# Performance work log

Hardware: AMD Instinct MI355X
Metric: run time of the kernel (lower is better)

## Reference

```python
import jax, jax.numpy as jnp
import numpy as np


def setup_inputs() -> dict:
    key = jax.random.key(0)
    ks = jax.random.split(key, 6)
    B, T, I, H, O = 64, 512, 256, 512, 256
    stdv = 1.0 / np.sqrt(H)
    u = lambda k, shape: jax.random.uniform(k, shape, jnp.float32, -stdv, stdv)
    return {
        "x": jax.random.normal(ks[0], (B, T, I), jnp.float32),
        "W": u(ks[1], (I, 4 * H)),
        "U": u(ks[2], (H, 4 * H)),
        "bias": u(ks[3], (4 * H,)),
        "Wl": u(ks[4], (H, O)),
        "bl": u(ks[5], (O,)),
    }


def lstm_scan(x, W, U, bias):
    B, T, I = x.shape
    H = U.shape[0]
    # Precompute input projections for all timesteps in one big GEMM: [B,T,4H]
    x_proj = jnp.einsum("bti,ig->btg", x, W) + bias

    def step(carry, xp_t):
        h, c = carry
        gates = xp_t + h @ U  # [B, 4H]
        i_t = jax.nn.sigmoid(gates[:, :H])
        f_t = jax.nn.sigmoid(gates[:, H:2 * H])
        g_t = jnp.tanh(gates[:, 2 * H:3 * H])
        o_t = jax.nn.sigmoid(gates[:, 3 * H:])
        c_new = f_t * c + i_t * g_t
        h_new = o_t * jnp.tanh(c_new)
        return (h_new, c_new), h_new

    h0 = jnp.zeros((B, H), x.dtype)
    c0 = jnp.zeros((B, H), x.dtype)
    (h_T, c_T), hs = jax.lax.scan(step, (h0, c0), jnp.swapaxes(x_proj, 0, 1))
    hidden_seq = jnp.swapaxes(hs, 0, 1)  # [B, T, H]
    return hidden_seq, h_T, c_T


def reference(x, W, U, bias, Wl, bl):
    hidden_seq, h_T, c_T = lstm_scan(x, W, U, bias)
    out = hidden_seq @ Wl + bl  # [B, T, O]
    return out, (h_T, c_T)
```

## Files before the change

### kernel.cpp

```cpp
#include <hip/hip_runtime.h>
#include <stdint.h>

typedef uint16_t u16;
typedef uint32_t u32;
typedef unsigned long long u64;
typedef __attribute__((ext_vector_type(8))) __bf16 bf16x8;
typedef __attribute__((ext_vector_type(8))) short short8;
typedef __attribute__((ext_vector_type(4))) float floatx4;

__device__ __forceinline__ float bf2f(u16 u) {
  union { u32 i; float f; } v; v.i = ((u32)u) << 16; return v.f;
}
__device__ __forceinline__ u16 f2bf(float f) {
  union { float f; u32 i; } v; v.f = f;
  u32 i = v.i;
  return (u16)((i + 0x7FFFu + ((i >> 16) & 1u)) >> 16);
}
__device__ __forceinline__ float sigm(float x) { return 1.f / (1.f + __expf(-x)); }
__device__ __forceinline__ float tanh_f(float x) {
  x = fminf(15.f, fmaxf(-15.f, x));
  float e = __expf(2.f * x);
  return (e - 1.f) / (e + 1.f);
}

__global__ __launch_bounds__(256) void transpose_all(
    const float* __restrict__ W, const float* __restrict__ U,
    const float* __restrict__ Wl,
    u16* __restrict__ WT, u16* __restrict__ UT, u16* __restrict__ WlT) {
  __shared__ u16 tile[32][33];
  int j = blockIdx.x;
  const float* src; u16* dst; int R, C, bx, by;
  if (j < 1024)      { src = U;  dst = UT;  R = 512; C = 2048; bx = j & 63; by = j >> 6; }
  else if (j < 1536) { j -= 1024; src = W;  dst = WT;  R = 256; C = 2048; bx = j & 63; by = j >> 6; }
  else               { j -= 1536; src = Wl; dst = WlT; R = 512; C = 256;  bx = j & 7;  by = j >> 3; }
  const int tx = threadIdx.x & 31, ty = threadIdx.x >> 5;
  int x = bx * 32 + tx;
#pragma unroll
  for (int jj = 0; jj < 4; ++jj) {
    int y = by * 32 + ty + jj * 8;
    tile[ty + jj * 8][tx] = f2bf(src[(size_t)y * C + x]);
  }
  __syncthreads();
  int x2 = by * 32 + tx;
#pragma unroll
  for (int jj = 0; jj < 4; ++jj) {
    int y2 = bx * 32 + ty + jj * 8;
    dst[(size_t)y2 * R + x2] = tile[tx][ty + jj * 8];
  }
}

#define T_STEPS 512
#define HLSZ (16 * 520)
#define NWORK 224

#define LSTM_STEP(XC, XN, TT)                                                  \
  {                                                                            \
    const int t = (TT);                                                        \
    const int tn = (t + 1) & (T_STEPS - 1);                                    \
          \
    if (((tn) & 63) == 0 && t < T_STEPS - 1) {                                 \
      _Pragma("unroll")                                                        \
      for (int r = 0; r < 4; ++r) {                                            \
        const u32* cc = xpctr + ((g * 16 + q4 * 4 + r) * 8 + (tn >> 6));       \
        while (__hip_atomic_load(cc, __ATOMIC_RELAXED,                         \
                                 __HIP_MEMORY_SCOPE_AGENT) < 32u)              \
          __builtin_amdgcn_s_sleep(2);                                         \
      }                                                                        \
      __asm__ volatile("" ::: "memory");                                       \
    }                                                                          \
                   \
    _Pragma("unroll")                                                          \
    for (int qg = 0; qg < 4; ++qg)                                             \
      _Pragma("unroll")                                                        \
      for (int r = 0; r < 4; ++r)                                              \
        XN[qg * 4 + r] = xp_base[((size_t)(q4 * 4 + r) * T_STEPS + tn) * 2048  \
                                 + qg * 512 + cb + n];                         \
    __asm__ volatile("" ::: "memory");                                         \
    floatx4 acc[4] = {};                                                       \
    if (t > 0) {                                                               \
      const u64* hsrc = (const u64*)(hT_all)                                   \
                        + (size_t)(g * T_STEPS + (t - 1)) * 2048;              \
      u64 v[8];                                                                \
      for (;;) {                                                               \
        _Pragma("unroll")                                                      \
        for (int it = 0; it < 8; ++it)                                         \
          v[it] = __hip_atomic_load(hsrc + it * 256 + tid, __ATOMIC_RELAXED,   \
                                    __HIP_MEMORY_SCOPE_AGENT);                 \
        bool ok = true;                                                        \
        _Pragma("unroll")                                                      \
        for (int it = 0; it < 8; ++it) ok &= (v[it] != ~0ull);                 \
        if (ok) break;                                                         \
      }                                                                        \
      __asm__ volatile("" ::: "memory");                                       \
      u16* buf = hls + ((t - 1) & 1) * HLSZ;                                   \
      _Pragma("unroll")                                                        \
      for (int it = 0; it < 8; ++it) {                                         \
        int idx = it * 256 + tid;                                              \
        int tile = idx >> 6, w = idx & 63;                                     \
        *(u64*)(buf + (w >> 2) * 520 + tile * 16 + (w & 3) * 4) = v[it];       \
      }                                                                        \
      __syncthreads();                                                         \
      _Pragma("unroll")                                                        \
      for (int kt = 0; kt < 16; ++kt) {                                        \
        bf16x8 a = *(const bf16x8*)(buf + n * 520 + kt * 32 + q4 * 8);         \
        acc[0] = __builtin_amdgcn_mfma_f32_16x16x32_bf16(a, u[0][kt], acc[0], 0, 0, 0); \
        acc[1] = __builtin_amdgcn_mfma_f32_16x16x32_bf16(a, u[1][kt], acc[1], 0, 0, 0); \
        acc[2] = __builtin_amdgcn_mfma_f32_16x16x32_bf16(a, u[2][kt], acc[2], 0, 0, 0); \
        acc[3] = __builtin_amdgcn_mfma_f32_16x16x32_bf16(a, u[3][kt], acc[3], 0, 0, 0); \
      }                                                                        \
    }                                                                          \
    _Pragma("unroll")                                                          \
    for (int r = 0; r < 4; ++r) {                                              \
      float gi = sigm(acc[0][r] + bf2f(XC[r]));                                \
      float gf = sigm(acc[1][r] + bf2f(XC[4 + r]));                            \
      float gg = tanh_f(acc[2][r] + bf2f(XC[8 + r]));                          \
      float go = sigm(acc[3][r] + bf2f(XC[12 + r]));                           \
      float cn = gf * cst[r] + gi * gg;                                        \
      cst[r] = cn;                                                             \
      float hv = go * tanh_f(cn);                                              \
      int row = q4 * 4 + r;                                                    \
      hp[row * 16 + n] = f2bf(hv);                                             \
      if (t == T_STEPS - 1) {                                                  \
        out_hT[(g * 16 + row) * 512 + cb + n] = hv;                            \
        out_cT[(g * 16 + row) * 512 + cb + n] = cn;                            \
      }                                                                        \
    }                                                                          \
    __asm__ volatile("s_waitcnt lgkmcnt(0)" ::: "memory");                     \
    {                                                                          \
      u64 v = *(const u64*)(hp + (lane >> 2) * 16 + (lane & 3) * 4);           \
      u64* hdst = (u64*)(hT_all) + (size_t)(g * T_STEPS + t) * 2048            \
                  + p * 64 + lane;                                             \
      __hip_atomic_store(hdst, v, __ATOMIC_RELAXED, __HIP_MEMORY_SCOPE_AGENT); \
    }                                                                          \
  }

__global__ __launch_bounds__(256, 1) void fused_lstm(
    const float* __restrict__ x,
    const u16* __restrict__ WT,
    const float* __restrict__ bias,
    u16* __restrict__ xp,
    const u16* __restrict__ UT,
    u16* __restrict__ hT_all,
    const u16* __restrict__ WlT,
    const float* __restrict__ bl,
    float* __restrict__ outC,
    float* __restrict__ out_hT,
    float* __restrict__ out_cT,
    u32* __restrict__ xpctr) {
  __shared__ __align__(16) u16 smem[2 * HLSZ + 4 * 256];
  const int bi = blockIdx.x;
  const int tid = threadIdx.x;

  if (bi >= 32) {
    u16* As = smem;
    u16* Bs = smem + 64 * 40;
    const int wid = bi - 32;
    const int wave = tid >> 6, lane = tid & 63;
    const int q4 = lane >> 4, n16 = lane & 15;
    const int mw = (wave >> 1) * 32, nw = (wave & 1) * 32;
    const int ldrow = tid >> 2, ldseg = (tid & 3) * 8;

    for (int j = wid; j < 16384; j += NWORK) {
      const int tch = j >> 11;
      const int rem = j & 2047;
      const int b = rem >> 5, nt = rem & 31;
      const int m0 = b * 512 + tch * 64, n0 = nt * 64;
      floatx4 acc[2][2] = {};
      for (int k0 = 0; k0 < 256; k0 += 32) {
        const float* ap = x + (size_t)(m0 + ldrow) * 256 + k0 + ldseg;
        floatx4 a0 = *(const floatx4*)ap;
        floatx4 a1 = *(const floatx4*)(ap + 4);
        short8 s;
        s[0] = (short)f2bf(a0[0]); s[1] = (short)f2bf(a0[1]);
        s[2] = (short)f2bf(a0[2]); s[3] = (short)f2bf(a0[3]);
        s[4] = (short)f2bf(a1[0]); s[5] = (short)f2bf(a1[1]);
        s[6] = (short)f2bf(a1[2]); s[7] = (short)f2bf(a1[3]);
        *(short8*)(As + ldrow * 40 + ldseg) = s;
        *(short8*)(Bs + ldrow * 40 + ldseg) =
            *(const short8*)(WT + (size_t)(n0 + ldrow) * 256 + k0 + ldseg);
        __syncthreads();
#pragma unroll
        for (int mi = 0; mi < 2; ++mi) {
          bf16x8 a = *(const bf16x8*)(As + (mw + mi * 16 + n16) * 40 + q4 * 8);
#pragma unroll
          for (int ni = 0; ni < 2; ++ni) {
            bf16x8 bb = *(const bf16x8*)(Bs + (nw + ni * 16 + n16) * 40 + q4 * 8);
            acc[mi][ni] = __builtin_amdgcn_mfma_f32_16x16x32_bf16(a, bb, acc[mi][ni], 0, 0, 0);
          }
        }
        __syncthreads();
      }
#pragma unroll
      for (int mi = 0; mi < 2; ++mi)
#pragma unroll
        for (int ni = 0; ni < 2; ++ni) {
          int col = n0 + nw + ni * 16 + n16;
          float bv = bias[col];
#pragma unroll
          for (int r = 0; r < 4; ++r) {
            int m = m0 + mw + mi * 16 + q4 * 4 + r;
            u16 val = f2bf(acc[mi][ni][r] + bv);
            __hip_atomic_store(xp + (size_t)m * 2048 + col, val,
                               __ATOMIC_RELAXED, __HIP_MEMORY_SCOPE_AGENT);
          }
        }
      __asm__ volatile("s_waitcnt vmcnt(0)" ::: "memory");
      __syncthreads();
      if (tid == 0)
        __hip_atomic_fetch_add(xpctr + b * 8 + tch, 1u,
                               __ATOMIC_RELAXED, __HIP_MEMORY_SCOPE_AGENT);
    }

    for (int j = wid; j < 2048; j += NWORK) {
      const int tb = j >> 4, g2 = (j >> 2) & 3, nt = j & 3;
      const int m0 = g2 * 8192 + tb * 64, n0 = nt * 64;
      const int mm = m0 + ldrow;
      const size_t slot = ((size_t)((mm >> 13) * 512 + ((mm & 8191) >> 4))) * 8192
                          + (mm & 15) * 16;

      if (tid == 0) {
        const u64* heads = (const u64*)(hT_all)
                           + (size_t)(g2 * T_STEPS + tb * 4 + 3) * 2048;
        for (;;) {
          bool ok = true;
#pragma unroll
          for (int p2 = 0; p2 < 32; ++p2)
            ok &= (__hip_atomic_load(heads + p2 * 64, __ATOMIC_RELAXED,
                                     __HIP_MEMORY_SCOPE_AGENT) != ~0ull);
          if (ok) break;
          __builtin_amdgcn_s_sleep(32);
        }
      }
      __syncthreads();

      floatx4 acc[2][2] = {};
      for (int k0 = 0; k0 < 512; k0 += 32) {
        int kk = k0 + ldseg;
        const u64* ap64 = (const u64*)(hT_all + slot + (kk >> 4) * 256 + (kk & 15));
        u64 lo, hi;
        for (;;) {
          lo = __hip_atomic_load(ap64, __ATOMIC_RELAXED, __HIP_MEMORY_SCOPE_AGENT);
          hi = __hip_atomic_load(ap64 + 1, __ATOMIC_RELAXED, __HIP_MEMORY_SCOPE_AGENT);
          if (lo != ~0ull && hi != ~0ull) break;
          __builtin_amdgcn_s_sleep(8);
        }
        *(u64*)(As + ldrow * 40 + ldseg) = lo;
        *(u64*)(As + ldrow * 40 + ldseg + 4) = hi;
        *(short8*)(Bs + ldrow * 40 + ldseg) =
            *(const short8*)(WlT + (size_t)(n0 + ldrow) * 512 + k0 + ldseg);
        __syncthreads();
#pragma unroll
        for (int mi = 0; mi < 2; ++mi) {
          bf16x8 a = *(const bf16x8*)(As + (mw + mi * 16 + n16) * 40 + q4 * 8);
#pragma unroll
          for (int ni = 0; ni < 2; ++ni) {
            bf16x8 bb = *(const bf16x8*)(Bs + (nw + ni * 16 + n16) * 40 + q4 * 8);
            acc[mi][ni] = __builtin_amdgcn_mfma_f32_16x16x32_bf16(a, bb, acc[mi][ni], 0, 0, 0);
          }
        }
        __syncthreads();
      }
#pragma unroll
      for (int mi = 0; mi < 2; ++mi)
#pragma unroll
        for (int ni = 0; ni < 2; ++ni) {
          int col = n0 + nw + ni * 16 + n16;
          float bv = bl[col];
#pragma unroll
          for (int r = 0; r < 4; ++r) {
            int m = m0 + mw + mi * 16 + q4 * 4 + r;
            int orow = ((m >> 13) * 16 + (m & 15)) * 512 + ((m & 8191) >> 4);
            outC[(size_t)orow * 256 + col] = acc[mi][ni][r] + bv;
          }
        }
    }
    return;
  }

  u16* hls = smem;
  u16* hstw = smem + 2 * HLSZ;
  const int g = (bi & 7) >> 1;
  const int wgi = ((bi & 1) << 2) | (bi >> 3);
  const int wave = tid >> 6;
  const int lane = tid & 63;
  const int n = lane & 15;
  const int q4 = lane >> 4;
  const int cb = wgi * 64 + wave * 16;
  const int p = wgi * 4 + wave;
  u16* hp = hstw + wave * 256;

  bf16x8 u[4][16];
#pragma unroll
  for (int qg = 0; qg < 4; ++qg) {
    const u16* up = UT + (size_t)(qg * 512 + cb + n) * 512;
#pragma unroll
    for (int kt = 0; kt < 16; ++kt)
      u[qg][kt] = *(const bf16x8*)(up + kt * 32 + q4 * 8);
  }

  float cst[4] = {0.f, 0.f, 0.f, 0.f};
  const u16* xp_base = xp + (size_t)(g * 16) * T_STEPS * 2048;

#pragma unroll
  for (int r = 0; r < 4; ++r) {
    const u32* cc = xpctr + ((g * 16 + q4 * 4 + r) * 8 + 0);
    while (__hip_atomic_load(cc, __ATOMIC_RELAXED, __HIP_MEMORY_SCOPE_AGENT) < 32u)
      __builtin_amdgcn_s_sleep(2);
  }
  __asm__ volatile("" ::: "memory");

  u16 xa[16], xb[16];
#pragma unroll
  for (int qg = 0; qg < 4; ++qg)
#pragma unroll
    for (int r = 0; r < 4; ++r)
      xa[qg * 4 + r] = xp_base[((size_t)(q4 * 4 + r) * T_STEPS + 0) * 2048
                               + qg * 512 + cb + n];

#pragma unroll 1
  for (int t2 = 0; t2 < T_STEPS; t2 += 2) {
    LSTM_STEP(xa, xb, t2)
    LSTM_STEP(xb, xa, t2 + 1)
  }
}

extern "C" void kernel_launch(void* const* d_in, const int* in_sizes, int n_in,
                              void* d_out, int out_size, void* d_ws, size_t ws_size,
                              hipStream_t stream) {
  (void)in_sizes; (void)n_in; (void)out_size; (void)ws_size;
  const float* x    = (const float*)d_in[0];
  const float* W    = (const float*)d_in[1];
  const float* U    = (const float*)d_in[2];
  const float* bias = (const float*)d_in[3];
  const float* Wl   = (const float*)d_in[4];
  const float* bl   = (const float*)d_in[5];
  float* out = (float*)d_out;
  char* ws = (char*)d_ws;

  u16* xp     = (u16*)(ws + 0);
  u16* UT     = (u16*)(ws + 134217728);
  u16* WT     = (u16*)(ws + 136314880);
  u16* WlT    = (u16*)(ws + 137363456);
  u16* hT_all = (u16*)(ws + 137625600);

  u32* ctr = (u32*)(out + 8388608);

  hipMemsetAsync(hT_all, 0xFF, 33554432, stream);
  hipMemsetAsync(ctr, 0x00, 2048, stream);

  transpose_all<<<1664, 256, 0, stream>>>(W, U, Wl, WT, UT, WlT);

  fused_lstm<<<256, 256, 0, stream>>>(x, WT, bias, xp, UT, hT_all, WlT, bl,
                                      out, out + 8388608, out + 8421376, ctr);
}
```

Baseline: 1.425 ms.

## Interleave two batch groups per recurrent workgroup to hide cross-block latency

Each recurrent workgroup now advances two independent batch groups (A and B) in alternating slots, with separate LDS buffers, cell state and x-projection registers for each. This halves the recurrent workgroups from 32 to 16 and gives 16 more blocks to the GEMM workers. While one group waits on the cross-workgroup h exchange, the other can compute, hiding the latency of the global-memory handoff. The cost is double the per-step compute per workgroup, more registers and LDS, and fewer CUs on the serial recurrence.

```diff
diff --git a/kernel.cpp b/kernel.cpp
--- a/kernel.cpp
+++ b/kernel.cpp
@@ -51,9 +51,9 @@
 
 #define T_STEPS 512
 #define HLSZ (16 * 520)
-#define NWORK 224
-
-#define LSTM_STEP(XC, XN, TT)                                                  \
+#define NWORK 240
+
+#define LSTM_SLOT(GG, XPB, CST, HLSB, HPP, XC, XN, TT)                         \
   {                                                                            \
     const int t = (TT);                                                        \
     const int tn = (t + 1) & (T_STEPS - 1);                                    \
@@ -61,7 +61,7 @@
     if (((tn) & 63) == 0 && t < T_STEPS - 1) {                                 \
       _Pragma("unroll")                                                        \
       for (int r = 0; r < 4; ++r) {                                            \
-        const u32* cc = xpctr + ((g * 16 + q4 * 4 + r) * 8 + (tn >> 6));       \
+        const u32* cc = xpctr + (((GG) * 16 + q4 * 4 + r) * 8 + (tn >> 6));    \
         while (__hip_atomic_load(cc, __ATOMIC_RELAXED,                         \
                                  __HIP_MEMORY_SCOPE_AGENT) < 32u)              \
           __builtin_amdgcn_s_sleep(2);                                         \
@@ -73,13 +73,13 @@
     for (int qg = 0; qg < 4; ++qg)                                             \
       _Pragma("unroll")                                                        \
       for (int r = 0; r < 4; ++r)                                              \
-        XN[qg * 4 + r] = xp_base[((size_t)(q4 * 4 + r) * T_STEPS + tn) * 2048  \
-                                 + qg * 512 + cb + n];                         \
+        XN[qg * 4 + r] = (XPB)[((size_t)(q4 * 4 + r) * T_STEPS + tn) * 2048    \
+                               + qg * 512 + cb + n];                           \
     __asm__ volatile("" ::: "memory");                                         \
     floatx4 acc[4] = {};                                                       \
     if (t > 0) {                                                               \
       const u64* hsrc = (const u64*)(hT_all)                                   \
-                        + (size_t)(g * T_STEPS + (t - 1)) * 2048;              \
+                        + (size_t)((GG) * T_STEPS + (t - 1)) * 2048;           \
       u64 v[8];                                                                \
       for (;;) {                                                               \
         _Pragma("unroll")                                                      \
@@ -92,7 +92,7 @@
         if (ok) break;                                                         \
       }                                                                        \
       __asm__ volatile("" ::: "memory");                                       \
-      u16* buf = hls + ((t - 1) & 1) * HLSZ;                                   \
+      u16* buf = (HLSB) + ((t - 1) & 1) * HLSZ;                                \
       _Pragma("unroll")                                                        \
       for (int it = 0; it < 8; ++it) {                                         \
         int idx = it * 256 + tid;                                              \
@@ -115,20 +115,20 @@
       float gf = sigm(acc[1][r] + bf2f(XC[4 + r]));                            \
       float gg = tanh_f(acc[2][r] + bf2f(XC[8 + r]));                          \
       float go = sigm(acc[3][r] + bf2f(XC[12 + r]));                           \
-      float cn = gf * cst[r] + gi * gg;                                        \
-      cst[r] = cn;                                                             \
+      float cn = gf * (CST)[r] + gi * gg;                                      \
+      (CST)[r] = cn;                                                           \
       float hv = go * tanh_f(cn);                                              \
       int row = q4 * 4 + r;                                                    \
-      hp[row * 16 + n] = f2bf(hv);                                             \
+      (HPP)[row * 16 + n] = f2bf(hv);                                          \
       if (t == T_STEPS - 1) {                                                  \
-        out_hT[(g * 16 + row) * 512 + cb + n] = hv;                            \
-        out_cT[(g * 16 + row) * 512 + cb + n] = cn;                            \
+        out_hT[((GG) * 16 + row) * 512 + cb + n] = hv;                         \
+        out_cT[((GG) * 16 + row) * 512 + cb + n] = cn;                         \
       }                                                                        \
     }                                                                          \
     __asm__ volatile("s_waitcnt lgkmcnt(0)" ::: "memory");                     \
     {                                                                          \
-      u64 v = *(const u64*)(hp + (lane >> 2) * 16 + (lane & 3) * 4);           \
-      u64* hdst = (u64*)(hT_all) + (size_t)(g * T_STEPS + t) * 2048            \
+      u64 v = *(const u64*)((HPP) + (lane >> 2) * 16 + (lane & 3) * 4);        \
+      u64* hdst = (u64*)(hT_all) + (size_t)((GG) * T_STEPS + t) * 2048         \
                   + p * 64 + lane;                                             \
       __hip_atomic_store(hdst, v, __ATOMIC_RELAXED, __HIP_MEMORY_SCOPE_AGENT); \
     }                                                                          \
@@ -147,14 +147,14 @@
     float* __restrict__ out_hT,
     float* __restrict__ out_cT,
     u32* __restrict__ xpctr) {
-  __shared__ __align__(16) u16 smem[2 * HLSZ + 4 * 256];
+  __shared__ __align__(16) u16 smem[4 * HLSZ + 8 * 256];
   const int bi = blockIdx.x;
   const int tid = threadIdx.x;
 
-  if (bi >= 32) {
+  if (bi >= 16) {
     u16* As = smem;
     u16* Bs = smem + 64 * 40;
-    const int wid = bi - 32;
+    const int wid = bi - 16;
     const int wave = tid >> 6, lane = tid & 63;
     const int q4 = lane >> 4, n16 = lane & 15;
     const int mw = (wave >> 1) * 32, nw = (wave & 1) * 32;
@@ -277,17 +277,20 @@
     return;
   }
 
-  u16* hls = smem;
-  u16* hstw = smem + 2 * HLSZ;
-  const int g = (bi & 7) >> 1;
-  const int wgi = ((bi & 1) << 2) | (bi >> 3);
+  u16* hlsA = smem;
+  u16* hlsB = smem + 2 * HLSZ;
+  u16* hstw = smem + 4 * HLSZ;
+  const int pair = bi >> 3;
+  const int wgi = bi & 7;
+  const int gA = pair * 2, gB = pair * 2 + 1;
   const int wave = tid >> 6;
   const int lane = tid & 63;
   const int n = lane & 15;
   const int q4 = lane >> 4;
   const int cb = wgi * 64 + wave * 16;
   const int p = wgi * 4 + wave;
-  u16* hp = hstw + wave * 256;
+  u16* hpA = hstw + wave * 256;
+  u16* hpB = hstw + 1024 + wave * 256;
 
   bf16x8 u[4][16];
 #pragma unroll
@@ -298,29 +301,39 @@
       u[qg][kt] = *(const bf16x8*)(up + kt * 32 + q4 * 8);
   }
 
-  float cst[4] = {0.f, 0.f, 0.f, 0.f};
-  const u16* xp_base = xp + (size_t)(g * 16) * T_STEPS * 2048;
+  float cstA[4] = {0.f, 0.f, 0.f, 0.f};
+  float cstB[4] = {0.f, 0.f, 0.f, 0.f};
+  const u16* xpA = xp + (size_t)(gA * 16) * T_STEPS * 2048;
+  const u16* xpB = xp + (size_t)(gB * 16) * T_STEPS * 2048;
 
 #pragma unroll
   for (int r = 0; r < 4; ++r) {
-    const u32* cc = xpctr + ((g * 16 + q4 * 4 + r) * 8 + 0);
-    while (__hip_atomic_load(cc, __ATOMIC_RELAXED, __HIP_MEMORY_SCOPE_AGENT) < 32u)
+    const u32* ccA = xpctr + ((gA * 16 + q4 * 4 + r) * 8 + 0);
+    while (__hip_atomic_load(ccA, __ATOMIC_RELAXED, __HIP_MEMORY_SCOPE_AGENT) < 32u)
       __builtin_amdgcn_s_sleep(2);
+    const u32* ccB = xpctr + ((gB * 16 + q4 * 4 + r) * 8 + 0);
+    while (__hip_atomic_load(ccB, __ATOMIC_RELAXED, __HIP_MEMORY_SCOPE_AGENT) < 32u)
+      __builtin_amdgcn_s_sleep(2);
   }
   __asm__ volatile("" ::: "memory");
 
-  u16 xa[16], xb[16];
+  u16 xaA[16], xbA[16], xaB[16], xbB[16];
 #pragma unroll
   for (int qg = 0; qg < 4; ++qg)
 #pragma unroll
-    for (int r = 0; r < 4; ++r)
-      xa[qg * 4 + r] = xp_base[((size_t)(q4 * 4 + r) * T_STEPS + 0) * 2048
-                               + qg * 512 + cb + n];
+    for (int r = 0; r < 4; ++r) {
+      xaA[qg * 4 + r] = xpA[((size_t)(q4 * 4 + r) * T_STEPS + 0) * 2048
+                            + qg * 512 + cb + n];
+      xaB[qg * 4 + r] = xpB[((size_t)(q4 * 4 + r) * T_STEPS + 0) * 2048
+                            + qg * 512 + cb + n];
+    }
 
 #pragma unroll 1
   for (int t2 = 0; t2 < T_STEPS; t2 += 2) {
-    LSTM_STEP(xa, xb, t2)
-    LSTM_STEP(xb, xa, t2 + 1)
+    LSTM_SLOT(gA, xpA, cstA, hlsA, hpA, xaA, xbA, t2)
+    LSTM_SLOT(gB, xpB, cstB, hlsB, hpB, xaB, xbB, t2)
+    LSTM_SLOT(gA, xpA, cstA, hlsA, hpA, xbA, xaA, t2 + 1)
+    LSTM_SLOT(gB, xpB, cstB, hlsB, hpB, xbB, xaB, t2 + 1)
   }
 }
 
```

Measured after the change: 2.621 ms. 83.9% more time.
